# Kernel tuning notes

Hardware: AMD Instinct MI355X
Metric: run time of the kernel (lower is better)

## Reference

```python
import jax, jax.numpy as jnp
import numpy as np

TEMP = 0.5
K_SEL = 20
NEG_SLOPE = 0.1


def setup_inputs() -> dict:
    key = jax.random.key(0)
    ks = jax.random.split(key, 12)
    B, N = 64, 20000
    F1, F2, D = 512, 256, 128
    init = lambda k, shape, fan: (jax.random.normal(k, shape) / np.sqrt(fan)).astype(jnp.float32)
    return {
        "patient_embedding": jax.random.normal(ks[0], (B, F1), dtype=jnp.float32),
        "gene_embedding": jax.random.normal(ks[1], (N, F2), dtype=jnp.float32),
        "Wq": init(ks[2], (F1, D), F1), "bq": jnp.zeros((D,), jnp.float32),
        "Wk": init(ks[3], (F2, D), F2), "bk": jnp.zeros((D,), jnp.float32),
        "Wv": init(ks[4], (F2, D), F2), "bv": jnp.zeros((D,), jnp.float32),
        "W1": init(ks[5], (2 * D, D), 2 * D), "b1": jnp.zeros((D,), jnp.float32),
        "w2": init(ks[6], (D,), D), "b2": jnp.zeros((), jnp.float32),
    }


def reference(patient_embedding, gene_embedding, Wq, bq, Wk, bk, Wv, bv, W1, b1, w2, b2):
    B = patient_embedding.shape[0]
    N = gene_embedding.shape[0]
    D = Wq.shape[1]

    Q = patient_embedding @ Wq + bq          # [B, D]
    Km = gene_embedding @ Wk + bk            # [N, D]
    V = gene_embedding @ Wv + bv             # [N, D]

    # MLP attention on cat([Q_exp, K_exp]); split W1 to avoid materializing [B,N,2D]
    q_part = Q @ W1[:D]                      # [B, D]
    k_part = Km @ W1[D:]                     # [N, D]
    h = jax.nn.leaky_relu(q_part[:, None, :] + k_part[None, :, :] + b1, NEG_SLOPE)  # [B, N, D]
    sim = h @ w2 + b2                        # [B, N]
    logits = sim / TEMP

    # gumbel-softmax, hard=True, independent noise per (b, k) row
    g = jax.random.gumbel(jax.random.key(42), (B, K_SEL, N), dtype=logits.dtype)
    y_soft = jax.nn.softmax((logits[:, None, :] + g) / TEMP, axis=-1)   # [B, K, N]
    y_hard = jax.nn.one_hot(jnp.argmax(y_soft, axis=-1), N, dtype=y_soft.dtype)
    masks = y_hard - jax.lax.stop_gradient(y_soft) + y_soft             # straight-through

    topk_values = jnp.einsum("bkn,nd->bkd", masks, V)                   # [B, K, D]
    scores = jnp.einsum("bd,bkd->bk", Q, topk_values) / np.sqrt(D).astype(np.float32)
    weights = jax.nn.softmax(scores, axis=-1)                           # [B, K] (dropout = eval/identity)
    context = jnp.einsum("bk,bkd->bd", weights, topk_values)            # [B, D]
    return context
```

## Files before the change

kernel.cpp:

```cpp
#include <hip/hip_runtime.h>

#define NG 20000

__device__ __forceinline__ void threefry2x32(unsigned x0, unsigned x1,
                                             unsigned& o0, unsigned& o1) {
  const unsigned ks0 = 0u;
  const unsigned ks1 = 42u;
  const unsigned ks2 = 0x1BD11BDAu ^ 0u ^ 42u;
  x0 += ks0; x1 += ks1;
#define TFR(r) { x0 += x1; x1 = (x1 << (r)) | (x1 >> (32 - (r))); x1 ^= x0; }
  TFR(13) TFR(15) TFR(26) TFR(6)
  x0 += ks1; x1 += ks2 + 1u;
  TFR(17) TFR(29) TFR(16) TFR(24)
  x0 += ks2; x1 += ks0 + 2u;
  TFR(13) TFR(15) TFR(26) TFR(6)
  x0 += ks0; x1 += ks1 + 3u;
  TFR(17) TFR(29) TFR(16) TFR(24)
  x0 += ks1; x1 += ks2 + 4u;
  TFR(13) TFR(15) TFR(26) TFR(6)
  x0 += ks2; x1 += ks0 + 5u;
#undef TFR
  o0 = x0; o1 = x1;
}

__device__ __forceinline__ unsigned tfbits(unsigned ctr) {
  unsigned o0, o1;
  threefry2x32(0u, ctr, o0, o1);
  return o0 ^ o1;
}

__device__ __forceinline__ float gumbel32(unsigned bits) {
  float f = __uint_as_float((bits >> 9) | 0x3f800000u) - 1.0f;
  float u = fmaxf(f, 1.17549435e-38f);
  const float l2u = __log2f(u);
  return fmaf(-0.69314718056f, __log2f(-l2u), 0.3665129206f);
}

__device__ __forceinline__ double gumbel64(unsigned bits) {
  float f = __uint_as_float((bits >> 9) | 0x3f800000u) - 1.0f;
  double u = (double)fmaxf(f, 1.17549435e-38f);
  return -log(-log(u));
}

__device__ __forceinline__ unsigned long long packcell(double v, int n) {
  unsigned long long u = (unsigned long long)__double_as_longlong(v);
  u = (u >> 63) ? ~u : (u | 0x8000000000000000ull);
  return (u & 0xFFFFFFFFFFFF8000ull) | (unsigned long long)(32767 - n);
}

__global__ __launch_bounds__(128) void kprep(
    const float* __restrict__ pe, const float* __restrict__ Wq,
    const float* __restrict__ bq, const float* __restrict__ Wk,
    const float* __restrict__ bk, const float* __restrict__ W1,
    const float* __restrict__ b1, const float* __restrict__ w2,
    float* __restrict__ Wf32, double* __restrict__ qbT,
    float* __restrict__ Qm, unsigned long long* __restrict__ cells,
    double2* __restrict__ c12) {
  __shared__ float L[512];
  __shared__ double Ld[128];
  const int t = threadIdx.x;
  const int bid = blockIdx.x;
  if (bid < 256) {
    L[t] = Wk[bid * 128 + t];
    __syncthreads();
    double acc = 0.0;
    #pragma unroll 16
    for (int j = 0; j < 128; ++j)
      acc = fma((double)L[j], (double)W1[(128 + j) * 128 + t], acc);
    Wf32[bid * 128 + t] = (float)acc;
  } else if (bid < 320) {
    const int b = bid - 256;
    #pragma unroll
    for (int i = 0; i < 4; ++i) L[t + 128 * i] = pe[b * 512 + t + 128 * i];
    __syncthreads();
    double q = (double)bq[t];
    #pragma unroll 16
    for (int f = 0; f < 512; ++f)
      q = fma((double)L[f], (double)Wq[f * 128 + t], q);
    Qm[b * 128 + t] = (float)q;
    Ld[t] = q;
    __syncthreads();
    double acc = (double)b1[t];
    #pragma unroll 8
    for (int j = 0; j < 128; ++j) {
      acc = fma(Ld[j], (double)W1[j * 128 + t], acc);
      acc = fma((double)bk[j], (double)W1[(128 + j) * 128 + t], acc);
    }
    qbT[t * 64 + b] = acc;
  } else {
    for (int i = t; i < 1280; i += 128) cells[i] = 0ull;
    const double w2d = (double)w2[t];
    c12[t] = make_double2(0.55 * w2d, 0.45 * w2d);
  }
}

__global__ __launch_bounds__(256) void kfused(
    const float* __restrict__ ge, const float* __restrict__ Wf32,
    const double* __restrict__ qbT, const double2* __restrict__ c12,
    unsigned long long* __restrict__ cells) {
  __shared__ double SBd[2048];
  __shared__ float kpL[2048];
  float* geL = (float*)SBd;
  float* simLf = (float*)SBd;
  const int t = threadIdx.x;
  const int wv = t >> 6;
  const int lane = t & 63;
  const int g0 = blockIdx.x * 16;

  {
    const float4* src = (const float4*)(ge + (size_t)g0 * 256);
    float4* dst = (float4*)geL;
    #pragma unroll
    for (int i = 0; i < 4; ++i) dst[t + i * 256] = src[t + i * 256];
  }
  __syncthreads();

  float acc[4][2];
  #pragma unroll
  for (int j = 0; j < 4; ++j) { acc[j][0] = 0.f; acc[j][1] = 0.f; }
  const float* wb0 = Wf32 + lane;
  const float* wb1 = Wf32 + lane + 64;
  const float* gL = geL + wv * 4 * 256;

  float wc0[4], wc1[4];
  #pragma unroll
  for (int ff = 0; ff < 4; ++ff) {
    wc0[ff] = wb0[ff * 128];
    wc1[ff] = wb1[ff * 128];
  }
  for (int f0 = 0; f0 < 256; f0 += 4) {
    float wn0[4], wn1[4];
    if (f0 < 252) {
      #pragma unroll
      for (int ff = 0; ff < 4; ++ff) {
        wn0[ff] = wb0[(f0 + 4 + ff) * 128];
        wn1[ff] = wb1[(f0 + 4 + ff) * 128];
      }
    }
    #pragma unroll
    for (int j = 0; j < 4; ++j) {
      const float4 gv = *(const float4*)(gL + j * 256 + f0);
      acc[j][0] = fmaf(gv.x, wc0[0], acc[j][0]);
      acc[j][1] = fmaf(gv.x, wc1[0], acc[j][1]);
      acc[j][0] = fmaf(gv.y, wc0[1], acc[j][0]);
      acc[j][1] = fmaf(gv.y, wc1[1], acc[j][1]);
      acc[j][0] = fmaf(gv.z, wc0[2], acc[j][0]);
      acc[j][1] = fmaf(gv.z, wc1[2], acc[j][1]);
      acc[j][0] = fmaf(gv.w, wc0[3], acc[j][0]);
      acc[j][1] = fmaf(gv.w, wc1[3], acc[j][1]);
    }
    #pragma unroll
    for (int ff = 0; ff < 4; ++ff) { wc0[ff] = wn0[ff]; wc1[ff] = wn1[ff]; }
  }

  __syncthreads();
  #pragma unroll
  for (int j = 0; j < 4; ++j) {
    kpL[(wv * 4 + j) * 128 + lane] = acc[j][0];
    kpL[(wv * 4 + j) * 128 + lane + 64] = acc[j][1];
  }
  __syncthreads();

  double s[4];
  #pragma unroll
  for (int j = 0; j < 4; ++j) s[j] = 0.0;
  for (int dd = 0; dd < 128; ++dd) {
    const double2 cc = c12[dd];
    const double qv = qbT[dd * 64 + lane];
    #pragma unroll
    for (int j = 0; j < 4; ++j) {
      const double kv = (double)kpL[(wv + j * 4) * 128 + dd];
      const double tt = qv + kv;
      s[j] = fma(tt, cc.x, s[j]);
      s[j] = fma(fabs(tt), cc.y, s[j]);
    }
  }
  #pragma unroll
  for (int j = 0; j < 4; ++j)
    simLf[lane * 17 + (wv + j * 4)] = (float)(2.0 * s[j]);
  __syncthreads();

  #pragma unroll
  for (int i = 0; i < 5; ++i) {
    const int cell = i * 256 + t;
    const int b = (unsigned)cell / 20u;
    const float* sb = simLf + b * 17;
    float m1 = -3e38f, m2 = -3e38f;
    int n1 = -1, n2 = -1;
    unsigned c1 = 0, c2 = 0;
    const unsigned ib = (unsigned)cell * 20000u + (unsigned)g0;
    #pragma unroll 4
    for (int g = 0; g < 16; ++g) {
      const unsigned bb = tfbits(ib + (unsigned)g);
      const float sc = sb[g] + gumbel32(bb);
      if (sc > m1) { m2 = m1; n2 = n1; c2 = c1; m1 = sc; n1 = g; c1 = bb; }
      else if (sc > m2) { m2 = sc; n2 = g; c2 = bb; }
    }
    unsigned long long pb =
        packcell((double)sb[n1] + gumbel64(c1), g0 + n1);
    if (n2 >= 0 && (m1 - m2) < 1e-4f) {
      const unsigned long long u2 =
          packcell((double)sb[n2] + gumbel64(c2), g0 + n2);
      if (u2 > pb) pb = u2;
    }
    atomicMax(&cells[cell], pb);
  }
}

__global__ __launch_bounds__(256) void kfinal(
    const float* __restrict__ ge, const float* __restrict__ Wv,
    const float* __restrict__ bv, const float* __restrict__ Qm,
    const unsigned long long* __restrict__ cells, float* __restrict__ out) {
  const int b = blockIdx.x;
  const int t = threadIdx.x;
  const int wv = t >> 6;
  const int lane = t & 63;
  __shared__ float sc[20];
  __shared__ float ctxp[4][128];
  const float2 qv = ((const float2*)(Qm + b * 128))[lane];
  const float2 bvv = ((const float2*)bv)[lane];
  const float* gr[5];
  float2 V[5];
  #pragma unroll
  for (int j = 0; j < 5; ++j) {
    const unsigned long long cell = cells[b * 20 + wv * 5 + j];
    const int n = 32767 - (int)(cell & 0x7FFFull);
    gr[j] = ge + (size_t)n * 256;
    V[j] = bvv;
  }
  for (int f = 0; f < 256; f += 4) {
    const float2 w0 = ((const float2*)(Wv + (size_t)(f + 0) * 128))[lane];
    const float2 w1 = ((const float2*)(Wv + (size_t)(f + 1) * 128))[lane];
    const float2 w2_ = ((const float2*)(Wv + (size_t)(f + 2) * 128))[lane];
    const float2 w3 = ((const float2*)(Wv + (size_t)(f + 3) * 128))[lane];
    #pragma unroll
    for (int j = 0; j < 5; ++j) {
      const float4 gv = *(const float4*)(gr[j] + f);
      V[j].x = fmaf(gv.x, w0.x, V[j].x); V[j].y = fmaf(gv.x, w0.y, V[j].y);
      V[j].x = fmaf(gv.y, w1.x, V[j].x); V[j].y = fmaf(gv.y, w1.y, V[j].y);
      V[j].x = fmaf(gv.z, w2_.x, V[j].x); V[j].y = fmaf(gv.z, w2_.y, V[j].y);
      V[j].x = fmaf(gv.w, w3.x, V[j].x); V[j].y = fmaf(gv.w, w3.y, V[j].y);
    }
  }
  #pragma unroll
  for (int j = 0; j < 5; ++j) {
    float pr = qv.x * V[j].x + qv.y * V[j].y;
    #pragma unroll
    for (int off = 32; off; off >>= 1) pr += __shfl_xor(pr, off, 64);
    if (lane == 0) sc[wv * 5 + j] = pr * 0.08838834764831845f;
  }
  __syncthreads();
  float m = -3.0e38f;
  #pragma unroll
  for (int i = 0; i < 20; ++i) m = fmaxf(m, sc[i]);
  float s = 0.f;
  #pragma unroll
  for (int i = 0; i < 20; ++i) s += expf(sc[i] - m);
  const float inv = 1.0f / s;
  float c0 = 0.f, c1 = 0.f;
  #pragma unroll
  for (int j = 0; j < 5; ++j) {
    const float wk = expf(sc[wv * 5 + j] - m) * inv;
    c0 = fmaf(wk, V[j].x, c0);
    c1 = fmaf(wk, V[j].y, c1);
  }
  ctxp[wv][2 * lane] = c0;
  ctxp[wv][2 * lane + 1] = c1;
  __syncthreads();
  if (t < 128)
    out[b * 128 + t] = (ctxp[0][t] + ctxp[1][t]) + (ctxp[2][t] + ctxp[3][t]);
}

extern "C" void kernel_launch(void* const* d_in, const int* in_sizes, int n_in,
                              void* d_out, int out_size, void* d_ws, size_t ws_size,
                              hipStream_t stream) {
  (void)in_sizes; (void)n_in; (void)out_size; (void)ws_size;
  const float* pe = (const float*)d_in[0];
  const float* ge = (const float*)d_in[1];
  const float* Wq = (const float*)d_in[2];
  const float* bq = (const float*)d_in[3];
  const float* Wk = (const float*)d_in[4];
  const float* bk = (const float*)d_in[5];
  const float* Wv = (const float*)d_in[6];
  const float* bvp = (const float*)d_in[7];
  const float* W1 = (const float*)d_in[8];
  const float* b1 = (const float*)d_in[9];
  const float* w2 = (const float*)d_in[10];

  char* w = (char*)d_ws;
  float* Wf32 = (float*)w;
  double* qbT = (double*)(w + 131072);
  float* Qm = (float*)(w + 196608);
  unsigned long long* cells =
      (unsigned long long*)(w + 229376);
  double2* c12 = (double2*)(w + 239616);
  float* out = (float*)d_out;

  kprep<<<dim3(321), dim3(128), 0, stream>>>(pe, Wq, bq, Wk, bk, W1, b1, w2,
                                             Wf32, qbT, Qm, cells, c12);
  kfused<<<dim3(1250), dim3(256), 0, stream>>>(ge, Wf32, qbT, c12, cells);
  kfinal<<<dim3(64), dim3(256), 0, stream>>>(ge, Wv, bvp, Qm, cells, out);
}
```

Baseline: 265.3 us.

## Halve genes per block in fused kernel and use alignbit for rotations

The fused projection/similarity/Gumbel kernel now handles 8 genes per block instead of 16, launches twice as many blocks and declares a higher occupancy target. Weights are read as float2 pairs, and the shared-memory footprint shrinks. The aim is more waves in flight to hide latency in the fp64 similarity loop and the threefry work. The trade-off is twice as many atomicMax updates to the selection cells and twice the per-block reloads of qbT and c12. The threefry rotate is also expressed through the alignbit intrinsic.

```diff
diff --git a/kernel.cpp b/kernel.cpp
--- a/kernel.cpp
+++ b/kernel.cpp
@@ -1,6 +1,10 @@
 #include <hip/hip_runtime.h>
 
 #define NG 20000
+
+__device__ __forceinline__ unsigned rotl32(unsigned x, int r) {
+  return __builtin_amdgcn_alignbit(x, x, 32 - r);
+}
 
 __device__ __forceinline__ void threefry2x32(unsigned x0, unsigned x1,
                                              unsigned& o0, unsigned& o1) {
@@ -8,7 +12,7 @@
   const unsigned ks1 = 42u;
   const unsigned ks2 = 0x1BD11BDAu ^ 0u ^ 42u;
   x0 += ks0; x1 += ks1;
-#define TFR(r) { x0 += x1; x1 = (x1 << (r)) | (x1 >> (32 - (r))); x1 ^= x0; }
+#define TFR(r) { x0 += x1; x1 = rotl32(x1, (r)); x1 ^= x0; }
   TFR(13) TFR(15) TFR(26) TFR(6)
   x0 += ks1; x1 += ks2 + 1u;
   TFR(17) TFR(29) TFR(16) TFR(24)
@@ -94,81 +98,71 @@
   }
 }
 
-__global__ __launch_bounds__(256) void kfused(
+__global__ __launch_bounds__(256, 8) void kfused(
     const float* __restrict__ ge, const float* __restrict__ Wf32,
     const double* __restrict__ qbT, const double2* __restrict__ c12,
     unsigned long long* __restrict__ cells) {
-  __shared__ double SBd[2048];
-  __shared__ float kpL[2048];
-  float* geL = (float*)SBd;
-  float* simLf = (float*)SBd;
+  __shared__ float SB[2048];
+  __shared__ float kpL[1024];
+  float* geL = SB;
+  float* simLf = SB;
   const int t = threadIdx.x;
   const int wv = t >> 6;
   const int lane = t & 63;
-  const int g0 = blockIdx.x * 16;
+  const int g0 = blockIdx.x * 8;
 
   {
     const float4* src = (const float4*)(ge + (size_t)g0 * 256);
     float4* dst = (float4*)geL;
-    #pragma unroll
-    for (int i = 0; i < 4; ++i) dst[t + i * 256] = src[t + i * 256];
-  }
-  __syncthreads();
-
-  float acc[4][2];
-  #pragma unroll
-  for (int j = 0; j < 4; ++j) { acc[j][0] = 0.f; acc[j][1] = 0.f; }
-  const float* wb0 = Wf32 + lane;
-  const float* wb1 = Wf32 + lane + 64;
-  const float* gL = geL + wv * 4 * 256;
-
-  float wc0[4], wc1[4];
-  #pragma unroll
-  for (int ff = 0; ff < 4; ++ff) {
-    wc0[ff] = wb0[ff * 128];
-    wc1[ff] = wb1[ff * 128];
-  }
+    dst[t] = src[t];
+    dst[t + 256] = src[t + 256];
+  }
+  __syncthreads();
+
+  float acc[2][2];
+  acc[0][0] = acc[0][1] = acc[1][0] = acc[1][1] = 0.f;
+  const float2* wb = (const float2*)Wf32 + lane;
+  const float* gL = geL + (wv * 2) * 256;
+
+  float2 wc[4];
+  #pragma unroll
+  for (int ff = 0; ff < 4; ++ff) wc[ff] = wb[ff * 64];
   for (int f0 = 0; f0 < 256; f0 += 4) {
-    float wn0[4], wn1[4];
+    float2 wn[4];
     if (f0 < 252) {
       #pragma unroll
-      for (int ff = 0; ff < 4; ++ff) {
-        wn0[ff] = wb0[(f0 + 4 + ff) * 128];
-        wn1[ff] = wb1[(f0 + 4 + ff) * 128];
-      }
-    }
-    #pragma unroll
-    for (int j = 0; j < 4; ++j) {
+      for (int ff = 0; ff < 4; ++ff) wn[ff] = wb[(f0 + 4 + ff) * 64];
+    }
+    #pragma unroll
+    for (int j = 0; j < 2; ++j) {
       const float4 gv = *(const float4*)(gL + j * 256 + f0);
-      acc[j][0] = fmaf(gv.x, wc0[0], acc[j][0]);
-      acc[j][1] = fmaf(gv.x, wc1[0], acc[j][1]);
-      acc[j][0] = fmaf(gv.y, wc0[1], acc[j][0]);
-      acc[j][1] = fmaf(gv.y, wc1[1], acc[j][1]);
-      acc[j][0] = fmaf(gv.z, wc0[2], acc[j][0]);
-      acc[j][1] = fmaf(gv.z, wc1[2], acc[j][1]);
-      acc[j][0] = fmaf(gv.w, wc0[3], acc[j][0]);
-      acc[j][1] = fmaf(gv.w, wc1[3], acc[j][1]);
-    }
-    #pragma unroll
-    for (int ff = 0; ff < 4; ++ff) { wc0[ff] = wn0[ff]; wc1[ff] = wn1[ff]; }
-  }
-
-  __syncthreads();
-  #pragma unroll
-  for (int j = 0; j < 4; ++j) {
-    kpL[(wv * 4 + j) * 128 + lane] = acc[j][0];
-    kpL[(wv * 4 + j) * 128 + lane + 64] = acc[j][1];
-  }
-  __syncthreads();
-
-  double s[4];
-  #pragma unroll
-  for (int j = 0; j < 4; ++j) s[j] = 0.0;
+      acc[j][0] = fmaf(gv.x, wc[0].x, acc[j][0]);
+      acc[j][1] = fmaf(gv.x, wc[0].y, acc[j][1]);
+      acc[j][0] = fmaf(gv.y, wc[1].x, acc[j][0]);
+      acc[j][1] = fmaf(gv.y, wc[1].y, acc[j][1]);
+      acc[j][0] = fmaf(gv.z, wc[2].x, acc[j][0]);
+      acc[j][1] = fmaf(gv.z, wc[2].y, acc[j][1]);
+      acc[j][0] = fmaf(gv.w, wc[3].x, acc[j][0]);
+      acc[j][1] = fmaf(gv.w, wc[3].y, acc[j][1]);
+    }
+    #pragma unroll
+    for (int ff = 0; ff < 4; ++ff) wc[ff] = wn[ff];
+  }
+
+  __syncthreads();
+  #pragma unroll
+  for (int j = 0; j < 2; ++j)
+    ((float2*)(kpL + (wv * 2 + j) * 128))[lane] =
+        make_float2(acc[j][0], acc[j][1]);
+  __syncthreads();
+
+  double s[2];
+  s[0] = 0.0; s[1] = 0.0;
   for (int dd = 0; dd < 128; ++dd) {
     const double2 cc = c12[dd];
     const double qv = qbT[dd * 64 + lane];
     #pragma unroll
-    for (int j = 0; j < 4; ++j) {
+    for (int j = 0; j < 2; ++j) {
       const double kv = (double)kpL[(wv + j * 4) * 128 + dd];
       const double tt = qv + kv;
       s[j] = fma(tt, cc.x, s[j]);
@@ -176,21 +170,21 @@
     }
   }
   #pragma unroll
-  for (int j = 0; j < 4; ++j)
-    simLf[lane * 17 + (wv + j * 4)] = (float)(2.0 * s[j]);
+  for (int j = 0; j < 2; ++j)
+    simLf[lane * 9 + (wv + j * 4)] = (float)(2.0 * s[j]);
   __syncthreads();
 
   #pragma unroll
   for (int i = 0; i < 5; ++i) {
     const int cell = i * 256 + t;
     const int b = (unsigned)cell / 20u;
-    const float* sb = simLf + b * 17;
+    const float* sb = simLf + b * 9;
     float m1 = -3e38f, m2 = -3e38f;
     int n1 = -1, n2 = -1;
     unsigned c1 = 0, c2 = 0;
     const unsigned ib = (unsigned)cell * 20000u + (unsigned)g0;
     #pragma unroll 4
-    for (int g = 0; g < 16; ++g) {
+    for (int g = 0; g < 8; ++g) {
       const unsigned bb = tfbits(ib + (unsigned)g);
       const float sc = sb[g] + gumbel32(bb);
       if (sc > m1) { m2 = m1; n2 = n1; c2 = c1; m1 = sc; n1 = g; c1 = bb; }
@@ -298,6 +292,6 @@
 
   kprep<<<dim3(321), dim3(128), 0, stream>>>(pe, Wq, bq, Wk, bk, W1, b1, w2,
                                              Wf32, qbT, Qm, cells, c12);
-  kfused<<<dim3(1250), dim3(256), 0, stream>>>(ge, Wf32, qbT, c12, cells);
+  kfused<<<dim3(2500), dim3(256), 0, stream>>>(ge, Wf32, qbT, c12, cells);
   kfinal<<<dim3(64), dim3(256), 0, stream>>>(ge, Wv, bvp, Qm, cells, out);
 }
```

Measured after the change: 325.6 us. 1.23x slower.
